# Kernel tuning notes

Measured on AMD Instinct MI355X. Metric: run time of the kernel, lower is better.

The kernel has to match this reference:

```python
import jax, jax.numpy as jnp
import numpy as np

DIM = 2304
H = 24
KVH = 8
HD = DIM // H          # 96
KV_DIM = KVH * HD      # 768
INNER = 6144           # int(2*4*2304/3) rounded to multiple of 256
B = 2
S = 2048
TEMB = 1024            # min(dim, 1024)
EPS = 1e-5
QK_EPS = 1e-5


def _rms(x, w, eps=EPS):
    return x * jax.lax.rsqrt(jnp.mean(x * x, axis=-1, keepdims=True) + eps) * w


def _rope(x, cos, sin):
    # x: (B, S, n_heads, HD); cos/sin: (S, HD//2); complex multiply on (even, odd) pairs
    xp = x.reshape(*x.shape[:-1], HD // 2, 2)
    x0, x1 = xp[..., 0], xp[..., 1]
    c = cos[None, :, None, :]
    s = sin[None, :, None, :]
    o0 = x0 * c - x1 * s
    o1 = x0 * s + x1 * c
    return jnp.stack([o0, o1], axis=-1).reshape(x.shape)


def setup_inputs() -> dict:
    key = jax.random.key(0)
    ks = jax.random.split(key, 16)
    std = 0.02
    return {
        "hidden_states": jax.random.normal(ks[0], (B, S, DIM), jnp.float32),
        "temb": jax.random.normal(ks[1], (B, TEMB), jnp.float32),
        "rope_cos": jnp.cos(jax.random.normal(ks[2], (S, HD // 2), jnp.float32)),
        "rope_sin": jnp.sin(jax.random.normal(ks[2], (S, HD // 2), jnp.float32)),
        "w_mod": jax.random.normal(ks[3], (TEMB, 4 * DIM), jnp.float32) * std,
        "b_mod": jnp.zeros((4 * DIM,), jnp.float32),
        "norm1_w": jnp.ones((DIM,), jnp.float32),
        "wq": jax.random.normal(ks[4], (DIM, DIM), jnp.float32) * std,
        "wk": jax.random.normal(ks[5], (DIM, KV_DIM), jnp.float32) * std,
        "wv": jax.random.normal(ks[6], (DIM, KV_DIM), jnp.float32) * std,
        "norm_q_w": jnp.ones((HD,), jnp.float32),
        "norm_k_w": jnp.ones((HD,), jnp.float32),
        "wo": jax.random.normal(ks[7], (DIM, DIM), jnp.float32) * std,
        "norm2_w": jnp.ones((DIM,), jnp.float32),
        "ffn_norm1_w": jnp.ones((DIM,), jnp.float32),
        "w1": jax.random.normal(ks[8], (DIM, INNER), jnp.float32) * std,
        "w2": jax.random.normal(ks[9], (INNER, DIM), jnp.float32) * std,
        "w3": jax.random.normal(ks[10], (DIM, INNER), jnp.float32) * std,
        "ffn_norm2_w": jnp.ones((DIM,), jnp.float32),
        "attention_mask": jnp.ones((B, S), jnp.bool_),
    }


def reference(hidden_states, temb, rope_cos, rope_sin, w_mod, b_mod, norm1_w,
              wq, wk, wv, norm_q_w, norm_k_w, wo, norm2_w, ffn_norm1_w,
              w1, w2, w3, ffn_norm2_w, attention_mask):
    b, s, _ = hidden_states.shape
    # LuminaRMSNormZero modulation
    emb = jax.nn.silu(temb) @ w_mod + b_mod
    scale_msa, gate_msa, scale_mlp, gate_mlp = jnp.split(emb, 4, axis=1)  # each (B, DIM)
    xn = _rms(hidden_states, norm1_w) * (1.0 + scale_msa[:, None, :])

    # GQA attention with QK RMSNorm + RoPE
    q = (xn @ wq).reshape(b, s, H, HD)
    k = (xn @ wk).reshape(b, s, KVH, HD)
    v = (xn @ wv).reshape(b, s, KVH, HD)
    q = _rms(q, norm_q_w, QK_EPS)
    k = _rms(k, norm_k_w, QK_EPS)
    q = _rope(q, rope_cos, rope_sin)
    k = _rope(k, rope_cos, rope_sin)
    n_rep = H // KVH
    k = jnp.repeat(k, n_rep, axis=2)  # (B,S,H,HD)
    v = jnp.repeat(v, n_rep, axis=2)
    scale = HD ** -0.5
    scores = jnp.einsum('bqhd,bkhd->bhqk', q, k) * scale
    mask = attention_mask.astype(bool)[:, None, None, :]
    scores = jnp.where(mask, scores, jnp.finfo(scores.dtype).min)
    probs = jax.nn.softmax(scores, axis=-1)
    attn = jnp.einsum('bhqk,bkhd->bqhd', probs, v).reshape(b, s, DIM)
    attn = attn @ wo

    x = hidden_states + jnp.tanh(gate_msa)[:, None, :] * _rms(attn, norm2_w)

    # SwiGLU FFN with scale modulation
    h = _rms(x, ffn_norm1_w) * (1.0 + scale_mlp[:, None, :])
    mlp = (jax.nn.silu(h @ w1) * (h @ w3)) @ w2
    return x + jnp.tanh(gate_mlp)[:, None, :] * _rms(mlp, ffn_norm2_w)
```

## Files before the change

### kernel.cpp

```cpp
#include <hip/hip_runtime.h>

typedef unsigned short ushort;
typedef __attribute__((ext_vector_type(8))) short short8;
typedef __attribute__((ext_vector_type(4))) float float4v;

__device__ __forceinline__ float b2f(ushort h) {
    unsigned int u = ((unsigned int)h) << 16;
    return __builtin_bit_cast(float, u);
}
__device__ __forceinline__ ushort f2bf(float f) {
    unsigned int u = __builtin_bit_cast(unsigned int, f);
    unsigned int r = u + 0x7fffu + ((u >> 16) & 1u);
    return (ushort)(r >> 16);
}
__device__ __forceinline__ float ldmix(const void* p, size_t i, int m) {
    return m ? ((const float*)p)[i] : b2f(((const ushort*)p)[i]);
}

__device__ __forceinline__ void gload16(const void* g, void* l) {
    __builtin_amdgcn_global_load_lds(
        (const __attribute__((address_space(1))) void*)(uintptr_t)g,
        (__attribute__((address_space(3))) void*)(unsigned int)(uintptr_t)l,
        16, 0, 0);
}

__device__ __forceinline__ float block_sum(float v) {
    __shared__ float sh[4];
    for (int off = 32; off; off >>= 1) v += __shfl_xor(v, off, 64);
    int lane = threadIdx.x & 63, w = threadIdx.x >> 6;
    if (lane == 0) sh[w] = v;
    __syncthreads();
    v = sh[0] + sh[1] + sh[2] + sh[3];
    __syncthreads();
    return v;
}

#define DIM   2304
#define H_Q   24
#define KVH   8
#define HD    96
#define KV_DIM 768
#define INNER 6144
#define S_LEN 2048
#define NTOK  4096
#define TEMB  1024
#define MODW  9216
#define QKVW  3840

__global__ void detect_mode(const unsigned* __restrict__ w, int* __restrict__ mode) {
    if (threadIdx.x == 0 && blockIdx.x == 0)
        mode[0] = ((w[0] & 0xFFFFu) == 0u) ? 1 : 0;
}

__global__ __launch_bounds__(256) void transpose_w(const void* __restrict__ src,
                                                   ushort* __restrict__ dst,
                                                   int R, int C, const int* __restrict__ md) {
    __shared__ ushort t[64][72];
    int m = md[0];
    int bx = blockIdx.x * 64;
    int by = blockIdx.y * 64;
    int x = threadIdx.x & 63;
    int y0 = threadIdx.x >> 6;
    if (m) {
        const float* s = (const float*)src;
        for (int yy = y0; yy < 64; yy += 4)
            t[yy][x] = f2bf(s[(size_t)(by + yy) * C + bx + x]);
    } else {
        const ushort* s = (const ushort*)src;
        for (int yy = y0; yy < 64; yy += 4)
            t[yy][x] = s[(size_t)(by + yy) * C + bx + x];
    }
    __syncthreads();
    for (int yy = y0; yy < 64; yy += 4)
        dst[(size_t)(bx + yy) * R + by + x] = t[x][yy];
}

__global__ __launch_bounds__(256) void mod_emb(const void* __restrict__ temb,
                                               const void* __restrict__ w_mod,
                                               const void* __restrict__ b_mod,
                                               float* __restrict__ emb,
                                               const int* __restrict__ md) {
    __shared__ float st[TEMB];
    int m = md[0];
    int b = blockIdx.y;
    int j = blockIdx.x * 256 + threadIdx.x;
    for (int k = threadIdx.x; k < TEMB; k += 256) {
        float t = ldmix(temb, b * TEMB + k, m);
        st[k] = t / (1.f + expf(-t));
    }
    __syncthreads();
    float s = 0.f;
    if (m) {
        const float* wm = (const float*)w_mod;
        for (int k = 0; k < TEMB; ++k) s += st[k] * wm[(size_t)k * MODW + j];
    } else {
        const ushort* wm = (const ushort*)w_mod;
        for (int k = 0; k < TEMB; ++k) s += st[k] * b2f(wm[(size_t)k * MODW + j]);
    }
    emb[b * MODW + j] = s + ldmix(b_mod, j, m);
}

__global__ __launch_bounds__(256) void rmsmod(const void* __restrict__ hid,
                                              const void* __restrict__ nw,
                                              const float* __restrict__ emb,
                                              ushort* __restrict__ xn,
                                              const int* __restrict__ md) {
    int m = md[0];
    int tok = blockIdx.x;
    int b = tok >> 11;
    float v[9]; float ss = 0.f;
    if (m) {
        const float* row = (const float*)hid + (size_t)tok * DIM;
        for (int i = 0; i < 9; ++i) { int d = threadIdx.x + i * 256; v[i] = row[d]; ss += v[i] * v[i]; }
    } else {
        const ushort* row = (const ushort*)hid + (size_t)tok * DIM;
        for (int i = 0; i < 9; ++i) { int d = threadIdx.x + i * 256; v[i] = b2f(row[d]); ss += v[i] * v[i]; }
    }
    ss = block_sum(ss);
    float rinv = rsqrtf(ss / (float)DIM + 1e-5f);
    for (int i = 0; i < 9; ++i) {
        int d = threadIdx.x + i * 256;
        float o = v[i] * rinv * ldmix(nw, d, m) * (1.f + emb[b * MODW + d]);
        xn[(size_t)tok * DIM + d] = f2bf(o);
    }
}


__device__ __forceinline__ void stage_ht(const ushort* __restrict__ G, int ldk,
                                         int row0, int k0, ushort* lbase, int t) {
    int tl = t ^ (((t >> 5) & 1) << 1);
#pragma unroll
    for (int rnd = 0; rnd < 2; ++rnd) {
        int lam = rnd * 512 + tl;
        int r = lam >> 3, c = lam & 7;
        gload16(G + (size_t)(row0 + r) * ldk + k0 + c * 8,
                lbase + ((size_t)(rnd * 512 + t)) * 8);
    }
}

__device__ __forceinline__ short8 ldsfrag(const ushort* b, int row, int kk, int quad) {
    int off = row * 128 + kk * 64 + quad * 16;
    off ^= ((off >> 9) & 1) << 5;
    return *(const short8*)((const char*)b + off);
}

#define VMWAIT(N) asm volatile("s_waitcnt vmcnt(" #N ")" ::: "memory")

#define DO_PHASE(SA, SB, Q, STAGE_CODE, WAIT_CODE)                              \
  do {                                                                          \
    if ((Q) == 0) {                                                             \
      _Pragma("unroll") for (int n = 0; n < 4; ++n) {                           \
        _Pragma("unroll") for (int kk = 0; kk < 2; ++kk)                        \
          bf[n][kk] = ldsfrag(SB, wn * 64 + n * 16 + lr, kk, quad);             \
      }                                                                         \
    }                                                                           \
    _Pragma("unroll") for (int mm = 0; mm < 2; ++mm) {                          \
      _Pragma("unroll") for (int kk = 0; kk < 2; ++kk)                          \
        af[mm][kk] = ldsfrag(SA, wm * 128 + ((Q) * 2 + mm) * 16 + lr, kk, quad);\
    }                                                                           \
    STAGE_CODE;                                                                 \
    WAIT_CODE;                                                                  \
    __builtin_amdgcn_s_barrier();                                               \
    asm volatile("s_waitcnt lgkmcnt(0)" ::: "memory");                          \
    __builtin_amdgcn_sched_barrier(0);                                          \
    __builtin_amdgcn_s_setprio(1);                                              \
    _Pragma("unroll") for (int kk = 0; kk < 2; ++kk) {                          \
      _Pragma("unroll") for (int mm = 0; mm < 2; ++mm) {                        \
        _Pragma("unroll") for (int n = 0; n < 4; ++n)                           \
          acc[(Q) * 2 + mm][n] = __builtin_amdgcn_mfma_f32_16x16x32_bf16(       \
              af[mm][kk], bf[n][kk], acc[(Q) * 2 + mm][n], 0, 0, 0);            \
      }                                                                         \
    }                                                                           \
    __builtin_amdgcn_s_setprio(0);                                              \
    __builtin_amdgcn_s_barrier();                                               \
  } while (0)

template <int EPI>
__global__ __launch_bounds__(512, 2) void gemm256(const ushort* __restrict__ A,
                                                  const ushort* __restrict__ Bt,
                                                  const ushort* other,
                                                  ushort* C, int N, int K) {
    __shared__ ushort sm[4][16384];
    int tid = threadIdx.x;
    int wave = tid >> 6, lane = tid & 63;
    int lr = lane & 15, quad = lane >> 4;
    int wm = wave >> 2, wn = wave & 3;

    int nwg = gridDim.x;
    int o = blockIdx.x;
    int wg = (o & 7) * (nwg >> 3) + (o >> 3);
    int gn = N >> 8;
    int bm = wg / gn, bn = wg - bm * gn;
    int am0 = bm << 8, bn0 = bn << 8;

    float4v acc[8][4];
#pragma unroll
    for (int m = 0; m < 8; ++m)
#pragma unroll
        for (int n = 0; n < 4; ++n)
#pragma unroll
            for (int r = 0; r < 4; ++r) acc[m][n][r] = 0.f;

    stage_ht(A,  K, am0,       0,  sm[0],        tid);
    stage_ht(A,  K, am0 + 128, 0,  &sm[0][8192], tid);
    stage_ht(Bt, K, bn0,       0,  sm[1],        tid);
    stage_ht(Bt, K, bn0 + 128, 0,  &sm[1][8192], tid);
    stage_ht(Bt, K, bn0,       64, sm[3],        tid);
    stage_ht(Bt, K, bn0 + 128, 64, &sm[3][8192], tid);
    VMWAIT(4);
    __builtin_amdgcn_s_barrier();

    short8 bf[4][2], af[2][2];
    int niter = K >> 7;
#pragma unroll 1
    for (int j = 0; j < niter; ++j) {
        int kb = j * 128 + 64;
        int kc = kb + 64;
        int kd = kc + 64;
        bool hc = kc < K;
        DO_PHASE(sm[0], sm[1], 0, stage_ht(A, K, am0,       kb, sm[2],        tid), ((void)0));
        DO_PHASE(sm[0], sm[1], 1, stage_ht(A, K, am0 + 128, kb, &sm[2][8192], tid), ((void)0));
        DO_PHASE(sm[0], sm[1], 2, if (hc) stage_ht(Bt, K, bn0,       kc, sm[1],        tid), ((void)0));
        DO_PHASE(sm[0], sm[1], 3, if (hc) stage_ht(Bt, K, bn0 + 128, kc, &sm[1][8192], tid),
                 if (hc) { VMWAIT(4); } else { VMWAIT(0); });
        DO_PHASE(sm[2], sm[3], 0, if (hc) stage_ht(A, K, am0,       kc, sm[0],        tid), ((void)0));
        DO_PHASE(sm[2], sm[3], 1, if (hc) stage_ht(A, K, am0 + 128, kc, &sm[0][8192], tid), ((void)0));
        DO_PHASE(sm[2], sm[3], 2, if (hc) stage_ht(Bt, K, bn0,       kd, sm[3],        tid), ((void)0));
        DO_PHASE(sm[2], sm[3], 3, if (hc) stage_ht(Bt, K, bn0 + 128, kd, &sm[3][8192], tid),
                 if (hc) { VMWAIT(4); } else { VMWAIT(0); });
    }

#pragma unroll
    for (int m = 0; m < 8; ++m)
#pragma unroll
        for (int n = 0; n < 4; ++n) {
            int row0 = am0 + wm * 128 + m * 16 + quad * 4;
            int col = bn0 + wn * 64 + n * 16 + lr;
#pragma unroll
            for (int r = 0; r < 4; ++r) {
                float v = acc[m][n][r];
                if (EPI == 1) v = v / (1.f + __expf(-v));
                if (EPI == 2) v = v * b2f(other[(size_t)(row0 + r) * N + col]);
                C[(size_t)(row0 + r) * N + col] = f2bf(v);
            }
        }
}

__global__ __launch_bounds__(256) void qkrope(ushort* __restrict__ x,
                                              const void* __restrict__ nw,
                                              const void* __restrict__ cosb,
                                              const void* __restrict__ sinb,
                                              int heads, const int* __restrict__ md,
                                              int rowstride, int coloff) {
    int m = md[0];
    int p = blockIdx.x * 4 + (threadIdx.x >> 6);
    int lane = threadIdx.x & 63;
    int tok = p / heads, hh = p - tok * heads;
    int sidx = tok & (S_LEN - 1);
    ushort* base = x + (size_t)tok * rowstride + coloff + hh * HD;
    float x0 = 0.f, x1 = 0.f;
    bool act = lane < 48;
    if (act) { x0 = b2f(base[2 * lane]); x1 = b2f(base[2 * lane + 1]); }
    float ss = x0 * x0 + x1 * x1;
    for (int off = 32; off; off >>= 1) ss += __shfl_xor(ss, off, 64);
    float rinv = rsqrtf(ss / (float)HD + 1e-5f);
    if (act) {
        float c = ldmix(cosb, sidx * 48 + lane, m);
        float s = ldmix(sinb, sidx * 48 + lane, m);
        float a0 = x0 * rinv * ldmix(nw, 2 * lane, m);
        float a1 = x1 * rinv * ldmix(nw, 2 * lane + 1, m);
        base[2 * lane]     = f2bf(a0 * c - a1 * s);
        base[2 * lane + 1] = f2bf(a0 * s + a1 * c);
    }
}

__global__ __launch_bounds__(256) void vtrans(const ushort* __restrict__ qkv,
                                              ushort* __restrict__ vt) {
    __shared__ ushort t[64][104];
    int st = blockIdx.x * 64;
    int bk = blockIdx.y;
    int b = bk >> 3, kvh = bk & 7;
    for (int idx = threadIdx.x; idx < 64 * 96; idx += 256) {
        int r = idx / 96, d = idx - r * 96;
        t[r][d] = qkv[(size_t)(b * S_LEN + st + r) * QKVW + (DIM + KV_DIM) + kvh * HD + d];
    }
    __syncthreads();
    for (int idx = threadIdx.x; idx < 96 * 64; idx += 256) {
        int d = idx >> 6, s2 = idx & 63;
        vt[((size_t)bk * HD + d) * S_LEN + st + s2] = t[s2][d];
    }
}

__global__ __launch_bounds__(256) void attn_kernel(const ushort* __restrict__ qkv,
                                                   const ushort* __restrict__ vt,
                                                   ushort* __restrict__ out) {
    __shared__ ushort Qs[64 * 104];
    __shared__ ushort Ks[64 * 104];
    __shared__ ushort Vs[96 * 72];
    __shared__ ushort Ps[4][16 * 72];
    int qb = blockIdx.x, head = blockIdx.y, b = blockIdx.z;
    int kvh = head / 3;
    int tid = threadIdx.x, wave = tid >> 6, lane = tid & 63;
    int lr = lane & 15, quad = lane >> 4;
    const float scale = 0.10206207261596575f;

    for (int idx = tid; idx < 64 * 96; idx += 256) {
        int r = idx / 96, d = idx - r * 96;
        Qs[r * 104 + d] = qkv[(size_t)(b * S_LEN + qb * 64 + r) * QKVW + head * HD + d];
    }
    __syncthreads();
    short8 aq[3];
#pragma unroll
    for (int ks = 0; ks < 3; ++ks)
        aq[ks] = *(const short8*)(&Qs[(wave * 16 + lr) * 104 + ks * 32 + quad * 8]);

    float4v O[6];
    for (int d = 0; d < 6; ++d) for (int r = 0; r < 4; ++r) O[d][r] = 0.f;
    float mrow[4], lacc[4];
    for (int r = 0; r < 4; ++r) { mrow[r] = -1e30f; lacc[r] = 0.f; }

    for (int kt = 0; kt < S_LEN / 64; ++kt) {
        int kbase = kt * 64;
        __syncthreads();
        for (int idx = tid; idx < 64 * 96; idx += 256) {
            int r = idx / 96, d = idx - r * 96;
            Ks[r * 104 + d] = qkv[(size_t)(b * S_LEN + kbase + r) * QKVW + DIM + kvh * HD + d];
        }
        for (int idx = tid; idx < 96 * 64; idx += 256) {
            int d = idx >> 6, c = idx & 63;
            Vs[d * 72 + c] = vt[((size_t)(b * KVH + kvh) * HD + d) * S_LEN + kbase + c];
        }
        __syncthreads();

        float4v S[4];
        for (int nb = 0; nb < 4; ++nb) for (int r = 0; r < 4; ++r) S[nb][r] = 0.f;
#pragma unroll
        for (int nb = 0; nb < 4; ++nb)
#pragma unroll
            for (int ks = 0; ks < 3; ++ks) {
                short8 bk_ = *(const short8*)(&Ks[(nb * 16 + lr) * 104 + ks * 32 + quad * 8]);
                S[nb] = __builtin_amdgcn_mfma_f32_16x16x32_bf16(aq[ks], bk_, S[nb], 0, 0, 0);
            }
#pragma unroll
        for (int nb = 0; nb < 4; ++nb)
#pragma unroll
            for (int r = 0; r < 4; ++r) S[nb][r] *= scale;

        float nm[4], alpha[4];
#pragma unroll
        for (int r = 0; r < 4; ++r) {
            float mx = fmaxf(fmaxf(S[0][r], S[1][r]), fmaxf(S[2][r], S[3][r]));
            for (int off = 1; off < 16; off <<= 1) mx = fmaxf(mx, __shfl_xor(mx, off, 64));
            nm[r] = fmaxf(mrow[r], mx);
            alpha[r] = __expf(mrow[r] - nm[r]);
            mrow[r] = nm[r];
        }
        float psum[4] = {0.f, 0.f, 0.f, 0.f};
#pragma unroll
        for (int nb = 0; nb < 4; ++nb)
#pragma unroll
            for (int r = 0; r < 4; ++r) {
                float p = __expf(S[nb][r] - nm[r]);
                psum[r] += p;
                Ps[wave][(quad * 4 + r) * 72 + nb * 16 + lr] = f2bf(p);
            }
#pragma unroll
        for (int r = 0; r < 4; ++r) {
            float s2 = psum[r];
            for (int off = 1; off < 16; off <<= 1) s2 += __shfl_xor(s2, off, 64);
            lacc[r] = lacc[r] * alpha[r] + s2;
        }
#pragma unroll
        for (int d = 0; d < 6; ++d)
#pragma unroll
            for (int r = 0; r < 4; ++r) O[d][r] *= alpha[r];
        __syncthreads();

        short8 pa[2];
#pragma unroll
        for (int ks = 0; ks < 2; ++ks)
            pa[ks] = *(const short8*)(&Ps[wave][lr * 72 + ks * 32 + quad * 8]);
#pragma unroll
        for (int db = 0; db < 6; ++db)
#pragma unroll
            for (int ks = 0; ks < 2; ++ks) {
                short8 bv = *(const short8*)(&Vs[(db * 16 + lr) * 72 + ks * 32 + quad * 8]);
                O[db] = __builtin_amdgcn_mfma_f32_16x16x32_bf16(pa[ks], bv, O[db], 0, 0, 0);
            }
    }
#pragma unroll
    for (int r = 0; r < 4; ++r) {
        float inv = 1.f / lacc[r];
        int row = b * S_LEN + qb * 64 + wave * 16 + quad * 4 + r;
#pragma unroll
        for (int db = 0; db < 6; ++db)
            out[(size_t)row * DIM + head * HD + db * 16 + lr] = f2bf(O[db][r] * inv);
    }
}

__global__ __launch_bounds__(256) void resid1(const void* __restrict__ hid,
                                              const ushort* __restrict__ ao,
                                              const void* __restrict__ n2w,
                                              const float* __restrict__ emb,
                                              ushort* __restrict__ x,
                                              const int* __restrict__ md) {
    int m = md[0];
    int tok = blockIdx.x;
    int b = tok >> 11;
    const ushort* row = ao + (size_t)tok * DIM;
    float v[9]; float ss = 0.f;
    for (int i = 0; i < 9; ++i) { int d = threadIdx.x + i * 256; v[i] = b2f(row[d]); ss += v[i] * v[i]; }
    ss = block_sum(ss);
    float rinv = rsqrtf(ss / (float)DIM + 1e-5f);
    for (int i = 0; i < 9; ++i) {
        int d = threadIdx.x + i * 256;
        float g = tanhf(emb[b * MODW + DIM + d]);
        float h = ldmix(hid, (size_t)tok * DIM + d, m);
        x[(size_t)tok * DIM + d] = f2bf(h + g * (v[i] * rinv * ldmix(n2w, d, m)));
    }
}

__global__ __launch_bounds__(256) void ffnnorm(const ushort* __restrict__ x,
                                               const void* __restrict__ nw,
                                               const float* __restrict__ emb,
                                               ushort* __restrict__ h,
                                               const int* __restrict__ md) {
    int m = md[0];
    int tok = blockIdx.x;
    int b = tok >> 11;
    const ushort* row = x + (size_t)tok * DIM;
    float v[9]; float ss = 0.f;
    for (int i = 0; i < 9; ++i) { int d = threadIdx.x + i * 256; v[i] = b2f(row[d]); ss += v[i] * v[i]; }
    ss = block_sum(ss);
    float rinv = rsqrtf(ss / (float)DIM + 1e-5f);
    for (int i = 0; i < 9; ++i) {
        int d = threadIdx.x + i * 256;
        h[(size_t)tok * DIM + d] = f2bf(v[i] * rinv * ldmix(nw, d, m) * (1.f + emb[b * MODW + 2 * DIM + d]));
    }
}

__global__ __launch_bounds__(256) void finalk(const ushort* __restrict__ x,
                                              const ushort* __restrict__ mlp,
                                              const void* __restrict__ nw,
                                              const float* __restrict__ emb,
                                              void* __restrict__ out,
                                              const int* __restrict__ md) {
    int m = md[0];
    int tok = blockIdx.x;
    int b = tok >> 11;
    const ushort* row = mlp + (size_t)tok * DIM;
    float v[9]; float ss = 0.f;
    for (int i = 0; i < 9; ++i) { int d = threadIdx.x + i * 256; v[i] = b2f(row[d]); ss += v[i] * v[i]; }
    ss = block_sum(ss);
    float rinv = rsqrtf(ss / (float)DIM + 1e-5f);
    for (int i = 0; i < 9; ++i) {
        int d = threadIdx.x + i * 256;
        float g = tanhf(emb[b * MODW + 3 * DIM + d]);
        float o = b2f(x[(size_t)tok * DIM + d]) + g * (v[i] * rinv * ldmix(nw, d, m));
        if (m) ((float*)out)[(size_t)tok * DIM + d] = o;
        else   ((ushort*)out)[(size_t)tok * DIM + d] = f2bf(o);
    }
}

extern "C" void kernel_launch(void* const* d_in, const int* in_sizes, int n_in,
                              void* d_out, int out_size, void* d_ws, size_t ws_size,
                              hipStream_t stream) {
    const void* hidden   = d_in[0];
    const void* temb     = d_in[1];
    const void* rope_cos = d_in[2];
    const void* rope_sin = d_in[3];
    const void* w_mod    = d_in[4];
    const void* b_mod    = d_in[5];
    const void* norm1_w  = d_in[6];
    const void* wq       = d_in[7];
    const void* wk       = d_in[8];
    const void* wv       = d_in[9];
    const void* norm_q_w = d_in[10];
    const void* norm_k_w = d_in[11];
    const void* wo       = d_in[12];
    const void* norm2_w  = d_in[13];
    const void* ffn1_w   = d_in[14];
    const void* w1       = d_in[15];
    const void* w2       = d_in[16];
    const void* w3       = d_in[17];
    const void* ffn2_w   = d_in[18];

    char* ws = (char*)d_ws;
    size_t off = 0;
    auto alloc = [&](size_t bytes) -> void* {
        void* p = ws + off;
        off += (bytes + 255) & ~(size_t)255;
        return p;
    };
    int*    md     = (int*)alloc(256);
    float*  emb    = (float*)alloc((size_t)2 * MODW * 4);
    ushort* warena = (ushort*)alloc((size_t)2 * DIM * INNER * 2);
    ushort* qkv    = (ushort*)alloc((size_t)NTOK * QKVW * 2);
    ushort* g      = (ushort*)alloc((size_t)NTOK * INNER * 2);
    ushort* act0   = (ushort*)alloc((size_t)NTOK * DIM * 2);
    ushort* act1   = (ushort*)alloc((size_t)NTOK * DIM * 2);
    ushort* vT     = (ushort*)alloc((size_t)NTOK * KV_DIM * 2);

    ushort* wqkvT = warena;
    ushort* wkT = warena + (size_t)DIM * DIM;
    ushort* wvT = wkT + (size_t)KV_DIM * DIM;
    ushort* woT = warena;
    ushort* w1T = warena;
    ushort* w3T = warena + (size_t)INNER * DIM;
    ushort* w2T = warena;

    ushort* xn   = act0;
    ushort* attn = act0;
    ushort* xbf  = act0;
    ushort* hbuf = act1;
    ushort* mlp  = act1;
    ushort* ao   = qkv;

    dim3 blk(256);
    dim3 blk512(512);

    detect_mode<<<1, 64, 0, stream>>>((const unsigned*)norm1_w, md);

    transpose_w<<<dim3(DIM / 64, DIM / 64), blk, 0, stream>>>(wq, wqkvT, DIM, DIM, md);
    transpose_w<<<dim3(KV_DIM / 64, DIM / 64), blk, 0, stream>>>(wk, wkT, DIM, KV_DIM, md);
    transpose_w<<<dim3(KV_DIM / 64, DIM / 64), blk, 0, stream>>>(wv, wvT, DIM, KV_DIM, md);

    mod_emb<<<dim3(MODW / 256, 2), blk, 0, stream>>>(temb, w_mod, b_mod, emb, md);
    rmsmod<<<NTOK, blk, 0, stream>>>(hidden, norm1_w, emb, xn, md);

    gemm256<0><<<dim3((NTOK / 256) * (QKVW / 256)), blk512, 0, stream>>>(
        xn, wqkvT, nullptr, qkv, QKVW, DIM);

    qkrope<<<NTOK * H_Q / 4, blk, 0, stream>>>(qkv, norm_q_w, rope_cos, rope_sin, H_Q, md, QKVW, 0);
    qkrope<<<NTOK * KVH / 4, blk, 0, stream>>>(qkv, norm_k_w, rope_cos, rope_sin, KVH, md, QKVW, DIM);
    vtrans<<<dim3(S_LEN / 64, 2 * KVH), blk, 0, stream>>>(qkv, vT);

    attn_kernel<<<dim3(S_LEN / 64, H_Q, 2), blk, 0, stream>>>(qkv, vT, attn);

    transpose_w<<<dim3(DIM / 64, DIM / 64), blk, 0, stream>>>(wo, woT, DIM, DIM, md);
    gemm256<0><<<dim3((NTOK / 256) * (DIM / 256)), blk512, 0, stream>>>(
        attn, woT, nullptr, ao, DIM, DIM);
    resid1<<<NTOK, blk, 0, stream>>>(hidden, ao, norm2_w, emb, xbf, md);

    transpose_w<<<dim3(INNER / 64, DIM / 64), blk, 0, stream>>>(w1, w1T, DIM, INNER, md);
    transpose_w<<<dim3(INNER / 64, DIM / 64), blk, 0, stream>>>(w3, w3T, DIM, INNER, md);
    ffnnorm<<<NTOK, blk, 0, stream>>>(xbf, ffn1_w, emb, hbuf, md);
    gemm256<1><<<dim3((NTOK / 256) * (INNER / 256)), blk512, 0, stream>>>(
        hbuf, w1T, nullptr, g, INNER, DIM);
    gemm256<2><<<dim3((NTOK / 256) * (INNER / 256)), blk512, 0, stream>>>(
        hbuf, w3T, g, g, INNER, DIM);

    transpose_w<<<dim3(DIM / 64, INNER / 64), blk, 0, stream>>>(w2, w2T, INNER, DIM, md);
    gemm256<0><<<dim3((NTOK / 256) * (DIM / 256)), blk512, 0, stream>>>(
        g, w2T, nullptr, mlp, DIM, INNER);
    finalk<<<NTOK, blk, 0, stream>>>(xbf, mlp, ffn2_w, emb, d_out, md);

    (void)in_sizes; (void)n_in; (void)out_size; (void)ws_size;
}
```

Baseline: 1.517 ms.

## Prefetch K/V tiles via registers and streamline online softmax in attention

The attention kernel now loads Q, K and V with 16-byte vector loads. The next K/V tile is prefetched into registers while the current tile is being computed, replacing the scalar per-element staging. The softmax scale times log2(e) is folded into Q during the RoPE pass, so the kernel can use exp2 directly and skip the per-element scale multiply. The running max is rescaled lazily, only when it grows by more than a threshold, and P is packed with a paired bf16 convert. A block-wide barrier is replaced by a wave-local LDS wait, and launch bounds request 3 blocks per CU, which adds register pressure and may cause spills.

```diff
diff --git a/kernel.cpp b/kernel.cpp
--- a/kernel.cpp
+++ b/kernel.cpp
@@ -46,6 +46,7 @@
 #define TEMB  1024
 #define MODW  9216
 #define QKVW  3840
+#define SCALE_L2E 0.14724444f
 
 __global__ void detect_mode(const unsigned* __restrict__ w, int* __restrict__ mode) {
     if (threadIdx.x == 0 && blockIdx.x == 0)
@@ -124,7 +125,6 @@
         xn[(size_t)tok * DIM + d] = f2bf(o);
     }
 }
-
 
 __device__ __forceinline__ void stage_ht(const ushort* __restrict__ G, int ldk,
                                          int row0, int k0, ushort* lbase, int t) {
@@ -251,7 +251,7 @@
                                               const void* __restrict__ cosb,
                                               const void* __restrict__ sinb,
                                               int heads, const int* __restrict__ md,
-                                              int rowstride, int coloff) {
+                                              int rowstride, int coloff, float oscale) {
     int m = md[0];
     int p = blockIdx.x * 4 + (threadIdx.x >> 6);
     int lane = threadIdx.x & 63;
@@ -269,8 +269,8 @@
         float s = ldmix(sinb, sidx * 48 + lane, m);
         float a0 = x0 * rinv * ldmix(nw, 2 * lane, m);
         float a1 = x1 * rinv * ldmix(nw, 2 * lane + 1, m);
-        base[2 * lane]     = f2bf(a0 * c - a1 * s);
-        base[2 * lane + 1] = f2bf(a0 * s + a1 * c);
+        base[2 * lane]     = f2bf((a0 * c - a1 * s) * oscale);
+        base[2 * lane + 1] = f2bf((a0 * s + a1 * c) * oscale);
     }
 }
 
@@ -291,9 +291,9 @@
     }
 }
 
-__global__ __launch_bounds__(256) void attn_kernel(const ushort* __restrict__ qkv,
-                                                   const ushort* __restrict__ vt,
-                                                   ushort* __restrict__ out) {
+__global__ __launch_bounds__(256, 3) void attn_kernel(const ushort* __restrict__ qkv,
+                                                      const ushort* __restrict__ vt,
+                                                      ushort* __restrict__ out) {
     __shared__ ushort Qs[64 * 104];
     __shared__ ushort Ks[64 * 104];
     __shared__ ushort Vs[96 * 72];
@@ -302,17 +302,36 @@
     int kvh = head / 3;
     int tid = threadIdx.x, wave = tid >> 6, lane = tid & 63;
     int lr = lane & 15, quad = lane >> 4;
-    const float scale = 0.10206207261596575f;
-
-    for (int idx = tid; idx < 64 * 96; idx += 256) {
-        int r = idx / 96, d = idx - r * 96;
-        Qs[r * 104 + d] = qkv[(size_t)(b * S_LEN + qb * 64 + r) * QKVW + head * HD + d];
+
+    int srow = wave * 16 + (lane >> 2);
+    int schk = (lane & 3) * 8;
+    int vrow0 = tid >> 3;
+    int vcol = (tid & 7) * 8;
+
+    {
+        const ushort* qg = qkv + (size_t)(b * S_LEN + qb * 64 + srow) * QKVW + head * HD + schk;
+        ushort* ql = Qs + srow * 104 + schk;
+#pragma unroll
+        for (int i = 0; i < 3; ++i)
+            *(short8*)(ql + i * 32) = *(const short8*)(qg + i * 32);
     }
     __syncthreads();
     short8 aq[3];
 #pragma unroll
     for (int ks = 0; ks < 3; ++ks)
         aq[ks] = *(const short8*)(&Qs[(wave * 16 + lr) * 104 + ks * 32 + quad * 8]);
+
+    const ushort* kg = qkv + (size_t)(b * S_LEN + srow) * QKVW + DIM + kvh * HD + schk;
+    const ushort* vg = vt + ((size_t)(b * KVH + kvh) * HD + vrow0) * S_LEN + vcol;
+    ushort* kl = Ks + srow * 104 + schk;
+    ushort* vl = Vs + vrow0 * 72 + vcol;
+
+    short8 kreg[3], vreg[3];
+#pragma unroll
+    for (int i = 0; i < 3; ++i) {
+        kreg[i] = *(const short8*)(kg + i * 32);
+        vreg[i] = *(const short8*)(vg + (size_t)i * 32 * S_LEN);
+    }
 
     float4v O[6];
     for (int d = 0; d < 6; ++d) for (int r = 0; r < 4; ++r) O[d][r] = 0.f;
@@ -320,17 +339,22 @@
     for (int r = 0; r < 4; ++r) { mrow[r] = -1e30f; lacc[r] = 0.f; }
 
     for (int kt = 0; kt < S_LEN / 64; ++kt) {
-        int kbase = kt * 64;
         __syncthreads();
-        for (int idx = tid; idx < 64 * 96; idx += 256) {
-            int r = idx / 96, d = idx - r * 96;
-            Ks[r * 104 + d] = qkv[(size_t)(b * S_LEN + kbase + r) * QKVW + DIM + kvh * HD + d];
-        }
-        for (int idx = tid; idx < 96 * 64; idx += 256) {
-            int d = idx >> 6, c = idx & 63;
-            Vs[d * 72 + c] = vt[((size_t)(b * KVH + kvh) * HD + d) * S_LEN + kbase + c];
+#pragma unroll
+        for (int i = 0; i < 3; ++i) {
+            *(short8*)(kl + i * 32) = kreg[i];
+            *(short8*)(vl + i * 2304) = vreg[i];
         }
         __syncthreads();
+        if (kt + 1 < S_LEN / 64) {
+            const ushort* kg2 = kg + (size_t)(kt + 1) * 64 * QKVW;
+            const ushort* vg2 = vg + (kt + 1) * 64;
+#pragma unroll
+            for (int i = 0; i < 3; ++i) {
+                kreg[i] = *(const short8*)(kg2 + i * 32);
+                vreg[i] = *(const short8*)(vg2 + (size_t)i * 32 * S_LEN);
+            }
+        }
 
         float4v S[4];
         for (int nb = 0; nb < 4; ++nb) for (int r = 0; r < 4; ++r) S[nb][r] = 0.f;
@@ -341,40 +365,55 @@
                 short8 bk_ = *(const short8*)(&Ks[(nb * 16 + lr) * 104 + ks * 32 + quad * 8]);
                 S[nb] = __builtin_amdgcn_mfma_f32_16x16x32_bf16(aq[ks], bk_, S[nb], 0, 0, 0);
             }
-#pragma unroll
-        for (int nb = 0; nb < 4; ++nb)
-#pragma unroll
-            for (int r = 0; r < 4; ++r) S[nb][r] *= scale;
-
-        float nm[4], alpha[4];
+
+        float mx[4];
 #pragma unroll
         for (int r = 0; r < 4; ++r) {
-            float mx = fmaxf(fmaxf(S[0][r], S[1][r]), fmaxf(S[2][r], S[3][r]));
-            for (int off = 1; off < 16; off <<= 1) mx = fmaxf(mx, __shfl_xor(mx, off, 64));
-            nm[r] = fmaxf(mrow[r], mx);
-            alpha[r] = __expf(mrow[r] - nm[r]);
-            mrow[r] = nm[r];
-        }
-        float psum[4] = {0.f, 0.f, 0.f, 0.f};
-#pragma unroll
-        for (int nb = 0; nb < 4; ++nb)
+            float m2 = fmaxf(fmaxf(S[0][r], S[1][r]), fmaxf(S[2][r], S[3][r]));
+#pragma unroll
+            for (int off = 1; off < 16; off <<= 1) m2 = fmaxf(m2, __shfl_xor(m2, off, 64));
+            mx[r] = m2;
+        }
+        bool grow = false;
+#pragma unroll
+        for (int r = 0; r < 4; ++r) grow = grow || (mx[r] > mrow[r] + 8.f);
+        if (__any(grow)) {
 #pragma unroll
             for (int r = 0; r < 4; ++r) {
-                float p = __expf(S[nb][r] - nm[r]);
-                psum[r] += p;
-                Ps[wave][(quad * 4 + r) * 72 + nb * 16 + lr] = f2bf(p);
+                float nm = fmaxf(mrow[r], mx[r]);
+                float al = __builtin_amdgcn_exp2f(mrow[r] - nm);
+                mrow[r] = nm;
+                lacc[r] *= al;
+#pragma unroll
+                for (int d = 0; d < 6; ++d) O[d][r] *= al;
             }
+        }
+        float psum[4];
+#pragma unroll
+        for (int r = 0; r < 4; ++r) {
+            float p0 = __builtin_amdgcn_exp2f(S[0][r] - mrow[r]);
+            float p1 = __builtin_amdgcn_exp2f(S[1][r] - mrow[r]);
+            float p2 = __builtin_amdgcn_exp2f(S[2][r] - mrow[r]);
+            float p3 = __builtin_amdgcn_exp2f(S[3][r] - mrow[r]);
+            psum[r] = (p0 + p1) + (p2 + p3);
+            unsigned u01, u23;
+            asm("v_cvt_pk_bf16_f32 %0, %1, %2" : "=v"(u01) : "v"(p0), "v"(p1));
+            asm("v_cvt_pk_bf16_f32 %0, %1, %2" : "=v"(u23) : "v"(p2), "v"(p3));
+            ushort* pr = &Ps[wave][(quad * 4 + r) * 72 + lr];
+            pr[0]  = (ushort)u01;
+            pr[16] = (ushort)(u01 >> 16);
+            pr[32] = (ushort)u23;
+            pr[48] = (ushort)(u23 >> 16);
+        }
 #pragma unroll
         for (int r = 0; r < 4; ++r) {
             float s2 = psum[r];
+#pragma unroll
             for (int off = 1; off < 16; off <<= 1) s2 += __shfl_xor(s2, off, 64);
-            lacc[r] = lacc[r] * alpha[r] + s2;
-        }
-#pragma unroll
-        for (int d = 0; d < 6; ++d)
-#pragma unroll
-            for (int r = 0; r < 4; ++r) O[d][r] *= alpha[r];
-        __syncthreads();
+            lacc[r] += s2;
+        }
+        asm volatile("s_waitcnt lgkmcnt(0)" ::: "memory");
+        __builtin_amdgcn_sched_barrier(0);
 
         short8 pa[2];
 #pragma unroll
@@ -531,8 +570,8 @@
     gemm256<0><<<dim3((NTOK / 256) * (QKVW / 256)), blk512, 0, stream>>>(
         xn, wqkvT, nullptr, qkv, QKVW, DIM);
 
-    qkrope<<<NTOK * H_Q / 4, blk, 0, stream>>>(qkv, norm_q_w, rope_cos, rope_sin, H_Q, md, QKVW, 0);
-    qkrope<<<NTOK * KVH / 4, blk, 0, stream>>>(qkv, norm_k_w, rope_cos, rope_sin, KVH, md, QKVW, DIM);
+    qkrope<<<NTOK * H_Q / 4, blk, 0, stream>>>(qkv, norm_q_w, rope_cos, rope_sin, H_Q, md, QKVW, 0, SCALE_L2E);
+    qkrope<<<NTOK * KVH / 4, blk, 0, stream>>>(qkv, norm_k_w, rope_cos, rope_sin, KVH, md, QKVW, DIM, 1.0f);
     vtrans<<<dim3(S_LEN / 64, 2 * KVH), blk, 0, stream>>>(qkv, vT);
 
     attn_kernel<<<dim3(S_LEN / 64, H_Q, 2), blk, 0, stream>>>(qkv, vT, attn);
```

After: 1.275 ms (median of 2 runs). -16.0%, faster.
